# Optimization experiments

Hardware: AMD Instinct MI355X
Metric: run time of the kernel (lower is better)

Reference implementation:

```python
import jax, jax.numpy as jnp
import numpy as np

HIDDEN = 1024
FFN = 4096
NUM_EXPERTS = 8
TOP_K = 2
BATCH, SEQ = 2, 2048


def setup_inputs() -> dict:
    key = jax.random.key(0)
    ks = jax.random.split(key, 6)
    s_h = 1.0 / np.sqrt(HIDDEN)
    s_f = 1.0 / np.sqrt(FFN)
    return {
        "hidden_states": jax.random.normal(ks[0], (BATCH, SEQ, HIDDEN), jnp.float32),
        "gate_w": jax.random.uniform(ks[1], (HIDDEN, NUM_EXPERTS), jnp.float32, -s_h, s_h),
        "gate_b": jax.random.uniform(ks[2], (NUM_EXPERTS,), jnp.float32, -s_h, s_h),
        "w1": jax.random.uniform(ks[3], (NUM_EXPERTS, HIDDEN, FFN), jnp.float32, -s_h, s_h),
        "w3": jax.random.uniform(ks[4], (NUM_EXPERTS, HIDDEN, FFN), jnp.float32, -s_h, s_h),
        "w2": jax.random.uniform(ks[5], (NUM_EXPERTS, FFN, HIDDEN), jnp.float32, -s_f, s_f),
    }


def reference(hidden_states, gate_w, gate_b, w1, w3, w2):
    B, S, D = hidden_states.shape
    T = B * S
    x = hidden_states.reshape(T, D)

    # Router: softmax in fp32, top-2, renormalize (matches torch source)
    logits = x @ gate_w + gate_b                       # [T, E]
    probs = jax.nn.softmax(logits.astype(jnp.float32), axis=-1)
    top_w, top_idx = jax.lax.top_k(probs, TOP_K)       # [T, 2]
    top_w = top_w / jnp.sum(top_w, axis=-1, keepdims=True)

    # Dense combine weights [T, E]: zero for unselected experts.
    combine = jnp.zeros((T, NUM_EXPERTS), jnp.float32)
    combine = combine.at[jnp.arange(T)[:, None], top_idx].set(top_w)
    combine = combine.astype(x.dtype)

    # Grouped SwiGLU expert MLPs (vectorized over experts, zero-weight tokens
    # contribute nothing after combine).
    h = jax.nn.silu(jnp.einsum('td,edf->tef', x, w1)) * jnp.einsum('td,edf->tef', x, w3)
    out_e = jnp.einsum('tef,efd->ted', h, w2)          # [T, E, D]
    out = jnp.einsum('ted,te->td', out_e, combine)     # weighted combine
    return out.reshape(B, S, D)
```

## Files before the change

### kernel.cpp

```cpp
#include <hip/hip_runtime.h>


#define NTOK 4096
#define HID  1024
#define FFN  4096
#define NE   8
#define CAP  10240
#define MAXT 72
#define MAXT256 40
#define NKT5 16

typedef __bf16 bf16x8 __attribute__((ext_vector_type(8)));
typedef float  f32x4  __attribute__((ext_vector_type(4)));

typedef __attribute__((address_space(3))) unsigned int       lds_uint;
typedef const __attribute__((address_space(1))) unsigned int glob_uint;

__device__ __forceinline__ unsigned short f2bf(float f) {
  union { float f; unsigned u; } v; v.f = f;
  return (unsigned short)((v.u + 0x7FFFu + ((v.u >> 16) & 1u)) >> 16);
}

__device__ __forceinline__ void gload16(const void* g, void* l) {
  __builtin_amdgcn_global_load_lds((glob_uint*)g, (lds_uint*)l, 16, 0, 0);
}

__global__ void k0_zero_cvt(const float* __restrict__ x,
                            unsigned short* __restrict__ xbf,
                            float* __restrict__ out,
                            int* __restrict__ counts) {
  int i = blockIdx.x * 256 + threadIdx.x;
  const float4* x4 = (const float4*)x;
  float4 v = x4[i];
  uint2 p;
  p.x = (unsigned)f2bf(v.x) | ((unsigned)f2bf(v.y) << 16);
  p.y = (unsigned)f2bf(v.z) | ((unsigned)f2bf(v.w) << 16);
  ((uint2*)xbf)[i] = p;
  ((float4*)out)[i] = make_float4(0.f, 0.f, 0.f, 0.f);
  if (i < NE) counts[i] = 0;
}

__global__ __launch_bounds__(256) void k1_transpose(
    const float* __restrict__ s0, unsigned short* __restrict__ d0,
    const float* __restrict__ s1, unsigned short* __restrict__ d1,
    int Rfull, int Cfull, int rg0, int cg0, int RW, int CW) {
  __shared__ unsigned short tile[64 * 72];
  int z = blockIdx.z;
  const float* src = (z < 8 ? s0 : s1) + (size_t)(z & 7) * Rfull * Cfull;
  unsigned short* dst = (z < 8 ? d0 : d1) + (size_t)(z & 7) * RW * CW;
  int c0 = blockIdx.x * 64;
  int r0 = blockIdx.y * 64;
  int t = threadIdx.x;
  int q = t >> 4, p = t & 15;

  const float4* s4 = (const float4*)(src + (size_t)(rg0 + r0 + 4 * q) * Cfull
                                     + cg0 + c0) + p;
  unsigned short v[4][4];
#pragma unroll
  for (int u = 0; u < 4; u++) {
    float4 xv = s4[(size_t)u * (Cfull >> 2)];
    v[u][0] = f2bf(xv.x); v[u][1] = f2bf(xv.y);
    v[u][2] = f2bf(xv.z); v[u][3] = f2bf(xv.w);
  }
#pragma unroll
  for (int j = 0; j < 4; j++) {
    ushort4 w = make_ushort4(v[0][j], v[1][j], v[2][j], v[3][j]);
    *(ushort4*)&tile[(4 * p + j) * 72 + 4 * q] = w;
  }
  __syncthreads();
  int b = t & 7;
#pragma unroll
  for (int vi = 0; vi < 2; vi++) {
    int c = (t >> 3) + 32 * vi;
    uint4 w = *(const uint4*)&tile[c * 72 + 8 * b];
    *(uint4*)(dst + (size_t)(c0 + c) * RW + r0 + 8 * b) = w;
  }
}

__global__ void k2_router(const float* __restrict__ x,
                          const float* __restrict__ gw,
                          const float* __restrict__ gb,
                          int* __restrict__ topi, float* __restrict__ topw,
                          int* __restrict__ counts) {
  int wid = threadIdx.x >> 6, lane = threadIdx.x & 63;
  int t = blockIdx.x * 4 + wid;
  const float4* x4 = (const float4*)(x + (size_t)t * HID);
  const float4* g4 = (const float4*)gw;
  float acc[8];
#pragma unroll
  for (int e = 0; e < 8; e++) acc[e] = 0.f;
#pragma unroll
  for (int i = 0; i < 4; i++) {
    float4 xv = x4[i * 64 + lane];
    int dbase = (i * 64 + lane) * 4;
    float xs[4] = {xv.x, xv.y, xv.z, xv.w};
#pragma unroll
    for (int j = 0; j < 4; j++) {
      float4 ga  = g4[(dbase + j) * 2];
      float4 gbv = g4[(dbase + j) * 2 + 1];
      acc[0] += xs[j] * ga.x;  acc[1] += xs[j] * ga.y;
      acc[2] += xs[j] * ga.z;  acc[3] += xs[j] * ga.w;
      acc[4] += xs[j] * gbv.x; acc[5] += xs[j] * gbv.y;
      acc[6] += xs[j] * gbv.z; acc[7] += xs[j] * gbv.w;
    }
  }
#pragma unroll
  for (int e = 0; e < 8; e++)
#pragma unroll
    for (int m = 1; m < 64; m <<= 1) acc[e] += __shfl_xor(acc[e], m);
  if (lane == 0) {
    float lg[8];
#pragma unroll
    for (int e = 0; e < 8; e++) lg[e] = acc[e] + gb[e];
    int i0 = 0; float m0 = lg[0];
#pragma unroll
    for (int e = 1; e < 8; e++) if (lg[e] > m0) { m0 = lg[e]; i0 = e; }
    int i1 = -1; float m1 = -1e30f;
#pragma unroll
    for (int e = 0; e < 8; e++) if (e != i0 && lg[e] > m1) { m1 = lg[e]; i1 = e; }
    float w0 = 1.f / (1.f + __expf(m1 - m0));
    topi[2 * t] = i0; topi[2 * t + 1] = i1;
    topw[2 * t] = w0; topw[2 * t + 1] = 1.f - w0;
    atomicAdd(&counts[i0], 1);
    atomicAdd(&counts[i1], 1);
  }
}

__global__ void k3_scan(const int* __restrict__ counts, int* offs, int* fill,
                        int* t128_e, int* t128_row, int* t256_e, int* t256_row,
                        int* sorted_tok, float* sorted_w) {
  if (threadIdx.x == 0) {
    int off = 0, t1 = 0, t2 = 0;
    for (int e = 0; e < NE; e++) {
      offs[e] = off; fill[e] = 0;
      int nt1 = (counts[e] + 127) >> 7;
      for (int j = 0; j < nt1; j++) { t128_e[t1] = e; t128_row[t1] = off + j * 128; t1++; }
      int nt2 = (counts[e] + 255) >> 8;
      for (int j = 0; j < nt2; j++) { t256_e[t2] = e; t256_row[t2] = off + j * 256; t2++; }
      off += nt2 * 256;
    }
    for (; t1 < MAXT; t1++)    { t128_e[t1] = -1; t128_row[t1] = 0; }
    for (; t2 < MAXT256; t2++) { t256_e[t2] = -1; t256_row[t2] = 0; }
  }
  for (int i = threadIdx.x; i < CAP; i += 256) { sorted_tok[i] = 0; sorted_w[i] = 0.f; }
}

__global__ void k4_scatter(const int* __restrict__ topi, const float* __restrict__ topw,
                           const int* __restrict__ offs, int* __restrict__ fill,
                           int* __restrict__ sorted_tok, float* __restrict__ sorted_w) {
  int t = blockIdx.x * 256 + threadIdx.x;
#pragma unroll
  for (int k = 0; k < 2; k++) {
    int e = topi[2 * t + k];
    int p = atomicAdd(&fill[e], 1);
    int s = offs[e] + p;
    sorted_tok[s] = t;
    sorted_w[s]   = topw[2 * t + k];
  }
}


#define STG2(SMN, HOFF, S0, S1, KN)                        \
  do {                                                     \
    gload16((S0) + (KN), (SMN) + (HOFF) + sd);             \
    gload16((S1) + (KN), (SMN) + (HOFF) + 4096u + sd);     \
  } while (0)

template<int CFC>
__global__ __launch_bounds__(512, 2) void k5_gemm_h8(
    const unsigned short* __restrict__ xbf,
    const unsigned short* __restrict__ w1t,
    const unsigned short* __restrict__ w3t,
    unsigned short* __restrict__ h,
    const int* __restrict__ t256_e, const int* __restrict__ t256_row,
    const int* __restrict__ sorted_tok, int FCdyn) {
  const int FC = CFC ? CFC : FCdyn;
  extern __shared__ unsigned short sm[];

  int nb  = gridDim.x;
  int bid = blockIdx.x;
  int nid = (bid & 7) * (nb >> 3) + (bid >> 3);
  int tile = nid % MAXT256;
  int nblk = nid / MAXT256;

  int e = t256_e[tile];
  if (e < 0) return;
  int row0 = t256_row[tile];
  int n0 = nblk * 128;
  int tid = threadIdx.x;

  int sr = tid >> 3;
  int cs = ((tid & 7) ^ (sr & 7)) * 8;
  const unsigned short* pA0 = xbf + (size_t)sorted_tok[row0 +       sr] * HID + cs;
  const unsigned short* pA1 = xbf + (size_t)sorted_tok[row0 +  64 + sr] * HID + cs;
  const unsigned short* pA2 = xbf + (size_t)sorted_tok[row0 + 128 + sr] * HID + cs;
  const unsigned short* pA3 = xbf + (size_t)sorted_tok[row0 + 192 + sr] * HID + cs;
  size_t rb0 = ((size_t)e * FC + n0 + sr) * HID + cs;
  size_t rb1 = rb0 + (size_t)64 * HID;
  const unsigned short* pB10 = w1t + rb0;
  const unsigned short* pB11 = w1t + rb1;
  const unsigned short* pB30 = w3t + rb0;
  const unsigned short* pB31 = w3t + rb1;
  unsigned sd = (unsigned)tid * 8u;

  int wid = tid >> 6, lane = tid & 63, lm = lane & 15, q = lane >> 4;
  int wr = wid >> 1, wc = wid & 1;
  unsigned aOff  = (unsigned)(wr * 64 + lm) * 64u;
  unsigned b1Off = 16384u + (unsigned)(wc * 64 + lm) * 64u;
  unsigned b3Off = 24576u + (unsigned)(wc * 64 + lm) * 64u;
  unsigned px0 = (unsigned)((q ^ (lm & 7)) * 8);
  unsigned px1 = (unsigned)(((4 + q) ^ (lm & 7)) * 8);

  f32x4 acc1[4][4] = {};
  f32x4 acc3[4][4] = {};
  bf16x8 af[4][2], bfr[2][2];

  {
    unsigned short* smn = sm;
    STG2(smn, 0u,     pA0,  pA1,  0);
    STG2(smn, 8192u,  pA2,  pA3,  0);
    STG2(smn, 16384u, pB10, pB11, 0);
    STG2(smn, 24576u, pB30, pB31, 0);
  }
  asm volatile("s_waitcnt vmcnt(2)" ::: "memory");
  __builtin_amdgcn_s_barrier();
  __builtin_amdgcn_sched_barrier(0);

#pragma unroll 1
  for (int kt = 0; kt < NKT5; kt++) {
    const unsigned short* smc = sm + ((kt & 1) ? 32768u : 0u);
    unsigned short*       smn = sm + ((kt & 1) ? 0u : 32768u);
    int kn = ((kt + 1) & (NKT5 - 1)) * 64;

#pragma unroll
    for (int ti = 0; ti < 4; ti++) {
      af[ti][0] = *(const bf16x8*)(smc + aOff + ti * 1024u + px0);
      af[ti][1] = *(const bf16x8*)(smc + aOff + ti * 1024u + px1);
    }
#pragma unroll
    for (int j = 0; j < 2; j++) {
      bfr[j][0] = *(const bf16x8*)(smc + b1Off + j * 1024u + px0);
      bfr[j][1] = *(const bf16x8*)(smc + b1Off + j * 1024u + px1);
    }
    STG2(smn, 0u, pA0, pA1, kn);
    __builtin_amdgcn_s_barrier();
    __builtin_amdgcn_sched_barrier(0);
    __builtin_amdgcn_s_setprio(1);
#pragma unroll
    for (int ti = 0; ti < 4; ti++)
#pragma unroll
      for (int j = 0; j < 2; j++) {
        acc1[ti][j] = __builtin_amdgcn_mfma_f32_16x16x32_bf16(af[ti][0], bfr[j][0], acc1[ti][j], 0, 0, 0);
        acc1[ti][j] = __builtin_amdgcn_mfma_f32_16x16x32_bf16(af[ti][1], bfr[j][1], acc1[ti][j], 0, 0, 0);
      }
    __builtin_amdgcn_s_setprio(0);

#pragma unroll
    for (int j = 0; j < 2; j++) {
      bfr[j][0] = *(const bf16x8*)(smc + b1Off + 2048u + j * 1024u + px0);
      bfr[j][1] = *(const bf16x8*)(smc + b1Off + 2048u + j * 1024u + px1);
    }
    STG2(smn, 8192u, pA2, pA3, kn);
    asm volatile("s_waitcnt vmcnt(4)" ::: "memory");
    __builtin_amdgcn_s_barrier();
    __builtin_amdgcn_sched_barrier(0);
    __builtin_amdgcn_s_setprio(1);
#pragma unroll
    for (int ti = 0; ti < 4; ti++)
#pragma unroll
      for (int j = 0; j < 2; j++) {
        acc1[ti][2 + j] = __builtin_amdgcn_mfma_f32_16x16x32_bf16(af[ti][0], bfr[j][0], acc1[ti][2 + j], 0, 0, 0);
        acc1[ti][2 + j] = __builtin_amdgcn_mfma_f32_16x16x32_bf16(af[ti][1], bfr[j][1], acc1[ti][2 + j], 0, 0, 0);
      }
    __builtin_amdgcn_s_setprio(0);

#pragma unroll
    for (int j = 0; j < 2; j++) {
      bfr[j][0] = *(const bf16x8*)(smc + b3Off + j * 1024u + px0);
      bfr[j][1] = *(const bf16x8*)(smc + b3Off + j * 1024u + px1);
    }
    STG2(smn, 16384u, pB10, pB11, kn);
    __builtin_amdgcn_s_barrier();
    __builtin_amdgcn_sched_barrier(0);
    __builtin_amdgcn_s_setprio(1);
#pragma unroll
    for (int ti = 0; ti < 4; ti++)
#pragma unroll
      for (int j = 0; j < 2; j++) {
        acc3[ti][j] = __builtin_amdgcn_mfma_f32_16x16x32_bf16(af[ti][0], bfr[j][0], acc3[ti][j], 0, 0, 0);
        acc3[ti][j] = __builtin_amdgcn_mfma_f32_16x16x32_bf16(af[ti][1], bfr[j][1], acc3[ti][j], 0, 0, 0);
      }
    __builtin_amdgcn_s_setprio(0);

#pragma unroll
    for (int j = 0; j < 2; j++) {
      bfr[j][0] = *(const bf16x8*)(smc + b3Off + 2048u + j * 1024u + px0);
      bfr[j][1] = *(const bf16x8*)(smc + b3Off + 2048u + j * 1024u + px1);
    }
    STG2(smn, 24576u, pB30, pB31, kn);
    asm volatile("s_waitcnt vmcnt(2)" ::: "memory");
    __builtin_amdgcn_s_barrier();
    __builtin_amdgcn_sched_barrier(0);
    __builtin_amdgcn_s_setprio(1);
#pragma unroll
    for (int ti = 0; ti < 4; ti++)
#pragma unroll
      for (int j = 0; j < 2; j++) {
        acc3[ti][2 + j] = __builtin_amdgcn_mfma_f32_16x16x32_bf16(af[ti][0], bfr[j][0], acc3[ti][2 + j], 0, 0, 0);
        acc3[ti][2 + j] = __builtin_amdgcn_mfma_f32_16x16x32_bf16(af[ti][1], bfr[j][1], acc3[ti][2 + j], 0, 0, 0);
      }
    __builtin_amdgcn_s_setprio(0);
  }
  asm volatile("s_waitcnt vmcnt(0)" ::: "memory");

#pragma unroll
  for (int ti = 0; ti < 4; ti++)
#pragma unroll
    for (int tj = 0; tj < 4; tj++)
#pragma unroll
      for (int r = 0; r < 4; r++) {
        float v1 = acc1[ti][tj][r];
        float v3 = acc3[ti][tj][r];
        float hv = (v1 / (1.f + __expf(-v1))) * v3;
        int grow = row0 + wr * 64 + ti * 16 + q * 4 + r;
        int gcol = n0 + wc * 64 + tj * 16 + lm;
        h[(size_t)grow * FC + gcol] = f2bf(hv);
      }
}

template<int CFC>
__global__ __launch_bounds__(256) void k6_gemm_out(
    const unsigned short* __restrict__ h,
    const unsigned short* __restrict__ w2t,
    float* __restrict__ out,
    const int* __restrict__ tile_e, const int* __restrict__ tile_row,
    const int* __restrict__ sorted_tok, const float* __restrict__ sorted_w,
    int FCdyn) {
  const int FC = CFC ? CFC : FCdyn;
  __shared__ unsigned short lsA[128 * 32];
  __shared__ unsigned short lsB[128 * 32];
  __shared__ int   toks[128];
  __shared__ float wts[128];

  int nbk  = (int)(gridDim.x * gridDim.y);
  int bidl = (int)(blockIdx.x + gridDim.x * blockIdx.y);
  int nidk = (bidl & 7) * (nbk >> 3) + (bidl >> 3);
  int tile = nidk % (int)gridDim.x;
  int yb   = nidk / (int)gridDim.x;

  int e = tile_e[tile];
  if (e < 0) return;
  int row0 = tile_row[tile];
  int n0 = yb * 128;
  int tid = threadIdx.x;

  if (tid < 128) { toks[tid] = sorted_tok[row0 + tid]; wts[tid] = sorted_w[row0 + tid]; }

  int kc = tid & 3, lr = tid >> 2;
  int g = (kc ^ ((lr >> 1) & 3)) * 8;
  const unsigned short* ga0 = h + (size_t)(row0 + lr) * FC + g;
  const unsigned short* ga1 = h + (size_t)(row0 + lr + 64) * FC + g;
  const unsigned short* gb0 = w2t + ((size_t)e * HID + n0 + lr) * FC + g;
  const unsigned short* gb1 = w2t + ((size_t)e * HID + n0 + lr + 64) * FC + g;
  unsigned short* la0 = lsA + tid * 8;
  unsigned short* la1 = lsA + (256 + tid) * 8;
  unsigned short* lb0 = lsB + tid * 8;
  unsigned short* lb1 = lsB + (256 + tid) * 8;

  int wid = tid >> 6, lane = tid & 63, lm = lane & 15, q = lane >> 4;
  int wr = wid >> 1, wc = wid & 1;
  int qs = (q ^ ((lm >> 1) & 3)) * 8;
  const unsigned short* As = lsA + (wr * 64 + lm) * 32 + qs;
  const unsigned short* Bs = lsB + (wc * 64 + lm) * 32 + qs;

  f32x4 acc[4][4] = {};

#pragma unroll 1
  for (int ks = 0; ks < FC / 32; ks++) {
    __syncthreads();
    int k0 = ks * 32;
    gload16(ga0 + k0, la0);
    gload16(ga1 + k0, la1);
    gload16(gb0 + k0, lb0);
    gload16(gb1 + k0, lb1);
    __syncthreads();
    bf16x8 a[4], b[4];
#pragma unroll
    for (int ti = 0; ti < 4; ti++) a[ti] = *(const bf16x8*)(As + ti * 512);
#pragma unroll
    for (int tj = 0; tj < 4; tj++) b[tj] = *(const bf16x8*)(Bs + tj * 512);
#pragma unroll
    for (int ti = 0; ti < 4; ti++)
#pragma unroll
      for (int tj = 0; tj < 4; tj++)
        acc[ti][tj] = __builtin_amdgcn_mfma_f32_16x16x32_bf16(a[ti], b[tj], acc[ti][tj], 0, 0, 0);
  }

#pragma unroll
  for (int ti = 0; ti < 4; ti++)
#pragma unroll
    for (int r = 0; r < 4; r++) {
      int lrow = wr * 64 + ti * 16 + q * 4 + r;
      float wt = wts[lrow];
      if (wt != 0.f) {
        int trow = toks[lrow];
#pragma unroll
        for (int tj = 0; tj < 4; tj++) {
          int gcol = n0 + wc * 64 + tj * 16 + lm;
          atomicAdd(&out[(size_t)trow * HID + gcol], acc[ti][tj][r] * wt);
        }
      }
    }
}

extern "C" void kernel_launch(void* const* d_in, const int* in_sizes, int n_in,
                              void* d_out, int out_size, void* d_ws, size_t ws_size,
                              hipStream_t stream) {
  const float* x  = (const float*)d_in[0];
  const float* gw = (const float*)d_in[1];
  const float* gb = (const float*)d_in[2];
  const float* w1 = (const float*)d_in[3];
  const float* w3 = (const float*)d_in[4];
  const float* w2 = (const float*)d_in[5];
  float* out = (float*)d_out;

  char* ws = (char*)d_ws;
  int*   counts     = (int*)(ws + 0);
  int*   fill       = (int*)(ws + 32);
  int*   offs       = (int*)(ws + 64);
  int*   t128_e     = (int*)(ws + 96);
  int*   t128_row   = (int*)(ws + 416);
  int*   t256_e     = (int*)(ws + 736);
  int*   t256_row   = (int*)(ws + 896);
  int*   topi       = (int*)(ws + 2048);
  float* topw       = (float*)(ws + 34816);
  int*   sorted_tok = (int*)(ws + 67584);
  float* sorted_w   = (float*)(ws + 108544);
  unsigned short* xbf = (unsigned short*)(ws + 149504);
  const size_t base = 8538112ull;

  int FC = FFN;
  while (FC > 128) {
    size_t W  = (size_t)NE * FC * HID * 2;
    size_t Hb = (size_t)CAP * FC * 2;
    if (base + 3 * W + Hb <= ws_size) break;
    FC >>= 1;
  }
  size_t W = (size_t)NE * FC * HID * 2;
  unsigned short* w1t  = (unsigned short*)(ws + base);
  unsigned short* w3t  = (unsigned short*)(ws + base + W);
  unsigned short* w2t  = (unsigned short*)(ws + base + 2 * W);
  unsigned short* hbuf = (unsigned short*)(ws + base + 3 * W);
  int nc = FFN / FC;

  static bool attr_set = false;
  if (!attr_set) {
    hipFuncSetAttribute((const void*)k5_gemm_h8<4096>, hipFuncAttributeMaxDynamicSharedMemorySize, 131072);
    hipFuncSetAttribute((const void*)k5_gemm_h8<2048>, hipFuncAttributeMaxDynamicSharedMemorySize, 131072);
    hipFuncSetAttribute((const void*)k5_gemm_h8<1024>, hipFuncAttributeMaxDynamicSharedMemorySize, 131072);
    hipFuncSetAttribute((const void*)k5_gemm_h8<0>,    hipFuncAttributeMaxDynamicSharedMemorySize, 131072);
    attr_set = true;
  }

  k0_zero_cvt<<<4096, 256, 0, stream>>>(x, xbf, out, counts);
  k2_router<<<1024, 256, 0, stream>>>(x, gw, gb, topi, topw, counts);
  k3_scan<<<1, 256, 0, stream>>>(counts, offs, fill, t128_e, t128_row,
                                 t256_e, t256_row, sorted_tok, sorted_w);
  k4_scatter<<<16, 256, 0, stream>>>(topi, topw, offs, fill, sorted_tok, sorted_w);

  for (int c = 0; c < nc; c++) {
    int c0 = c * FC;
    k1_transpose<<<dim3(FC / 64, HID / 64, 16), 256, 0, stream>>>(
        w1, w1t, w3, w3t, HID, FFN, 0, c0, HID, FC);
    k1_transpose<<<dim3(HID / 64, FC / 64, 8), 256, 0, stream>>>(
        w2, w2t, nullptr, nullptr, FFN, HID, c0, 0, FC, HID);
    dim3 g5(MAXT256 * (FC / 128));
    if (FC == 4096) {
      k5_gemm_h8<4096><<<g5, 512, 131072, stream>>>(
          xbf, w1t, w3t, hbuf, t256_e, t256_row, sorted_tok, FC);
      k6_gemm_out<4096><<<dim3(MAXT, HID / 128), 256, 0, stream>>>(
          hbuf, w2t, out, t128_e, t128_row, sorted_tok, sorted_w, FC);
    } else if (FC == 2048) {
      k5_gemm_h8<2048><<<g5, 512, 131072, stream>>>(
          xbf, w1t, w3t, hbuf, t256_e, t256_row, sorted_tok, FC);
      k6_gemm_out<2048><<<dim3(MAXT, HID / 128), 256, 0, stream>>>(
          hbuf, w2t, out, t128_e, t128_row, sorted_tok, sorted_w, FC);
    } else if (FC == 1024) {
      k5_gemm_h8<1024><<<g5, 512, 131072, stream>>>(
          xbf, w1t, w3t, hbuf, t256_e, t256_row, sorted_tok, FC);
      k6_gemm_out<1024><<<dim3(MAXT, HID / 128), 256, 0, stream>>>(
          hbuf, w2t, out, t128_e, t128_row, sorted_tok, sorted_w, FC);
    } else {
      k5_gemm_h8<0><<<g5, 512, 131072, stream>>>(
          xbf, w1t, w3t, hbuf, t256_e, t256_row, sorted_tok, FC);
      k6_gemm_out<0><<<dim3(MAXT, HID / 128), 256, 0, stream>>>(
          hbuf, w2t, out, t128_e, t128_row, sorted_tok, sorted_w, FC);
    }
  }
}
```

Measured before the change: 871.1 us.

## Rewrite down-projection GEMM as 256x256 double-buffered 8-wave pipelined kernel

Replaces the 128x128 single-buffered down-projection kernel with a 512-thread kernel that computes a 256-row by 256-column output tile. It reuses the k5 style: double-buffered LDS in 64-wide K steps, staged global-to-LDS loads interleaved with MFMA phases, and setprio around the MFMA blocks. Each wave owns two 128-column halves through two accumulator sets. The aim is more data reuse per loaded byte and overlap of memory loads with MFMA work, at the cost of higher register and LDS use (128KB dynamic) and coarser tiles. Routing tables with 256-row tiles can waste more work on padded rows.

```diff
diff --git a/kernel.cpp b/kernel.cpp
--- a/kernel.cpp
+++ b/kernel.cpp
@@ -329,72 +329,155 @@
 }
 
 template<int CFC>
-__global__ __launch_bounds__(256) void k6_gemm_out(
+__global__ __launch_bounds__(512, 2) void k6_gemm_o8(
     const unsigned short* __restrict__ h,
     const unsigned short* __restrict__ w2t,
     float* __restrict__ out,
-    const int* __restrict__ tile_e, const int* __restrict__ tile_row,
+    const int* __restrict__ t256_e, const int* __restrict__ t256_row,
     const int* __restrict__ sorted_tok, const float* __restrict__ sorted_w,
     int FCdyn) {
   const int FC = CFC ? CFC : FCdyn;
-  __shared__ unsigned short lsA[128 * 32];
-  __shared__ unsigned short lsB[128 * 32];
-  __shared__ int   toks[128];
-  __shared__ float wts[128];
-
-  int nbk  = (int)(gridDim.x * gridDim.y);
-  int bidl = (int)(blockIdx.x + gridDim.x * blockIdx.y);
-  int nidk = (bidl & 7) * (nbk >> 3) + (bidl >> 3);
-  int tile = nidk % (int)gridDim.x;
-  int yb   = nidk / (int)gridDim.x;
-
-  int e = tile_e[tile];
+  const int NKT = FC / 64;
+  extern __shared__ unsigned short sm[];
+  __shared__ int   toks[256];
+  __shared__ float wts[256];
+
+  int nb  = gridDim.x;
+  int bid = blockIdx.x;
+  int nid = (bid & 7) * (nb >> 3) + (bid >> 3);
+  int tile = nid % MAXT256;
+  int nblk = nid / MAXT256;
+
+  int e = t256_e[tile];
   if (e < 0) return;
-  int row0 = tile_row[tile];
-  int n0 = yb * 128;
+  int row0 = t256_row[tile];
+  int n0 = nblk * 256;
   int tid = threadIdx.x;
 
-  if (tid < 128) { toks[tid] = sorted_tok[row0 + tid]; wts[tid] = sorted_w[row0 + tid]; }
-
-  int kc = tid & 3, lr = tid >> 2;
-  int g = (kc ^ ((lr >> 1) & 3)) * 8;
-  const unsigned short* ga0 = h + (size_t)(row0 + lr) * FC + g;
-  const unsigned short* ga1 = h + (size_t)(row0 + lr + 64) * FC + g;
-  const unsigned short* gb0 = w2t + ((size_t)e * HID + n0 + lr) * FC + g;
-  const unsigned short* gb1 = w2t + ((size_t)e * HID + n0 + lr + 64) * FC + g;
-  unsigned short* la0 = lsA + tid * 8;
-  unsigned short* la1 = lsA + (256 + tid) * 8;
-  unsigned short* lb0 = lsB + tid * 8;
-  unsigned short* lb1 = lsB + (256 + tid) * 8;
+  if (tid < 256) { toks[tid] = sorted_tok[row0 + tid]; wts[tid] = sorted_w[row0 + tid]; }
+
+  int sr = tid >> 3;
+  int cs = ((tid & 7) ^ (sr & 7)) * 8;
+  const unsigned short* pA0 = h + (size_t)(row0 +       sr) * FC + cs;
+  const unsigned short* pA1 = h + (size_t)(row0 +  64 + sr) * FC + cs;
+  const unsigned short* pA2 = h + (size_t)(row0 + 128 + sr) * FC + cs;
+  const unsigned short* pA3 = h + (size_t)(row0 + 192 + sr) * FC + cs;
+  size_t rb = ((size_t)e * HID + n0 + sr) * FC + cs;
+  const unsigned short* pB10 = w2t + rb;
+  const unsigned short* pB11 = w2t + rb + (size_t)64  * FC;
+  const unsigned short* pB30 = w2t + rb + (size_t)128 * FC;
+  const unsigned short* pB31 = w2t + rb + (size_t)192 * FC;
+  unsigned sd = (unsigned)tid * 8u;
 
   int wid = tid >> 6, lane = tid & 63, lm = lane & 15, q = lane >> 4;
   int wr = wid >> 1, wc = wid & 1;
-  int qs = (q ^ ((lm >> 1) & 3)) * 8;
-  const unsigned short* As = lsA + (wr * 64 + lm) * 32 + qs;
-  const unsigned short* Bs = lsB + (wc * 64 + lm) * 32 + qs;
-
-  f32x4 acc[4][4] = {};
+  unsigned aOff  = (unsigned)(wr * 64 + lm) * 64u;
+  unsigned b1Off = 16384u + (unsigned)(wc * 64 + lm) * 64u;
+  unsigned b3Off = 24576u + (unsigned)(wc * 64 + lm) * 64u;
+  unsigned px0 = (unsigned)((q ^ (lm & 7)) * 8);
+  unsigned px1 = (unsigned)(((4 + q) ^ (lm & 7)) * 8);
+
+  f32x4 acc1[4][4] = {};
+  f32x4 acc3[4][4] = {};
+  bf16x8 af[4][2], bfr[2][2];
+
+  {
+    unsigned short* smn = sm;
+    STG2(smn, 0u,     pA0,  pA1,  0);
+    STG2(smn, 8192u,  pA2,  pA3,  0);
+    STG2(smn, 16384u, pB10, pB11, 0);
+    STG2(smn, 24576u, pB30, pB31, 0);
+  }
+  asm volatile("s_waitcnt vmcnt(2)" ::: "memory");
+  __builtin_amdgcn_s_barrier();
+  __builtin_amdgcn_sched_barrier(0);
 
 #pragma unroll 1
-  for (int ks = 0; ks < FC / 32; ks++) {
-    __syncthreads();
-    int k0 = ks * 32;
-    gload16(ga0 + k0, la0);
-    gload16(ga1 + k0, la1);
-    gload16(gb0 + k0, lb0);
-    gload16(gb1 + k0, lb1);
-    __syncthreads();
-    bf16x8 a[4], b[4];
-#pragma unroll
-    for (int ti = 0; ti < 4; ti++) a[ti] = *(const bf16x8*)(As + ti * 512);
-#pragma unroll
-    for (int tj = 0; tj < 4; tj++) b[tj] = *(const bf16x8*)(Bs + tj * 512);
-#pragma unroll
-    for (int ti = 0; ti < 4; ti++)
-#pragma unroll
-      for (int tj = 0; tj < 4; tj++)
-        acc[ti][tj] = __builtin_amdgcn_mfma_f32_16x16x32_bf16(a[ti], b[tj], acc[ti][tj], 0, 0, 0);
-  }
+  for (int kt = 0; kt < NKT; kt++) {
+    const unsigned short* smc = sm + ((kt & 1) ? 32768u : 0u);
+    unsigned short*       smn = sm + ((kt & 1) ? 0u : 32768u);
+    int kn = (kt + 1 == NKT ? 0 : kt + 1) * 64;
+
+#pragma unroll
+    for (int ti = 0; ti < 4; ti++) {
+      af[ti][0] = *(const bf16x8*)(smc + aOff + ti * 1024u + px0);
+      af[ti][1] = *(const bf16x8*)(smc + aOff + ti * 1024u + px1);
+    }
+#pragma unroll
+    for (int j = 0; j < 2; j++) {
+      bfr[j][0] = *(const bf16x8*)(smc + b1Off + j * 1024u + px0);
+      bfr[j][1] = *(const bf16x8*)(smc + b1Off + j * 1024u + px1);
+    }
+    STG2(smn, 0u, pA0, pA1, kn);
+    __builtin_amdgcn_s_barrier();
+    __builtin_amdgcn_sched_barrier(0);
+    __builtin_amdgcn_s_setprio(1);
+#pragma unroll
+    for (int ti = 0; ti < 4; ti++)
+#pragma unroll
+      for (int j = 0; j < 2; j++) {
+        acc1[ti][j] = __builtin_amdgcn_mfma_f32_16x16x32_bf16(af[ti][0], bfr[j][0], acc1[ti][j], 0, 0, 0);
+        acc1[ti][j] = __builtin_amdgcn_mfma_f32_16x16x32_bf16(af[ti][1], bfr[j][1], acc1[ti][j], 0, 0, 0);
+      }
+    __builtin_amdgcn_s_setprio(0);
+
+#pragma unroll
+    for (int j = 0; j < 2; j++) {
+      bfr[j][0] = *(const bf16x8*)(smc + b1Off + 2048u + j * 1024u + px0);
+      bfr[j][1] = *(const bf16x8*)(smc + b1Off + 2048u + j * 1024u + px1);
+    }
+    STG2(smn, 8192u, pA2, pA3, kn);
+    asm volatile("s_waitcnt vmcnt(4)" ::: "memory");
+    __builtin_amdgcn_s_barrier();
+    __builtin_amdgcn_sched_barrier(0);
+    __builtin_amdgcn_s_setprio(1);
+#pragma unroll
+    for (int ti = 0; ti < 4; ti++)
+#pragma unroll
+      for (int j = 0; j < 2; j++) {
+        acc1[ti][2 + j] = __builtin_amdgcn_mfma_f32_16x16x32_bf16(af[ti][0], bfr[j][0], acc1[ti][2 + j], 0, 0, 0);
+        acc1[ti][2 + j] = __builtin_amdgcn_mfma_f32_16x16x32_bf16(af[ti][1], bfr[j][1], acc1[ti][2 + j], 0, 0, 0);
+      }
+    __builtin_amdgcn_s_setprio(0);
+
+#pragma unroll
+    for (int j = 0; j < 2; j++) {
+      bfr[j][0] = *(const bf16x8*)(smc + b3Off + j * 1024u + px0);
+      bfr[j][1] = *(const bf16x8*)(smc + b3Off + j * 1024u + px1);
+    }
+    STG2(smn, 16384u, pB10, pB11, kn);
+    __builtin_amdgcn_s_barrier();
+    __builtin_amdgcn_sched_barrier(0);
+    __builtin_amdgcn_s_setprio(1);
+#pragma unroll
+    for (int ti = 0; ti < 4; ti++)
+#pragma unroll
+      for (int j = 0; j < 2; j++) {
+        acc3[ti][j] = __builtin_amdgcn_mfma_f32_16x16x32_bf16(af[ti][0], bfr[j][0], acc3[ti][j], 0, 0, 0);
+        acc3[ti][j] = __builtin_amdgcn_mfma_f32_16x16x32_bf16(af[ti][1], bfr[j][1], acc3[ti][j], 0, 0, 0);
+      }
+    __builtin_amdgcn_s_setprio(0);
+
+#pragma unroll
+    for (int j = 0; j < 2; j++) {
+      bfr[j][0] = *(const bf16x8*)(smc + b3Off + 2048u + j * 1024u + px0);
+      bfr[j][1] = *(const bf16x8*)(smc + b3Off + 2048u + j * 1024u + px1);
+    }
+    STG2(smn, 24576u, pB30, pB31, kn);
+    asm volatile("s_waitcnt vmcnt(2)" ::: "memory");
+    __builtin_amdgcn_s_barrier();
+    __builtin_amdgcn_sched_barrier(0);
+    __builtin_amdgcn_s_setprio(1);
+#pragma unroll
+    for (int ti = 0; ti < 4; ti++)
+#pragma unroll
+      for (int j = 0; j < 2; j++) {
+        acc3[ti][2 + j] = __builtin_amdgcn_mfma_f32_16x16x32_bf16(af[ti][0], bfr[j][0], acc3[ti][2 + j], 0, 0, 0);
+        acc3[ti][2 + j] = __builtin_amdgcn_mfma_f32_16x16x32_bf16(af[ti][1], bfr[j][1], acc3[ti][2 + j], 0, 0, 0);
+      }
+    __builtin_amdgcn_s_setprio(0);
+  }
+  asm volatile("s_waitcnt vmcnt(0)" ::: "memory");
 
 #pragma unroll
   for (int ti = 0; ti < 4; ti++)
@@ -407,7 +490,8 @@
 #pragma unroll
         for (int tj = 0; tj < 4; tj++) {
           int gcol = n0 + wc * 64 + tj * 16 + lm;
-          atomicAdd(&out[(size_t)trow * HID + gcol], acc[ti][tj][r] * wt);
+          atomicAdd(&out[(size_t)trow * HID + gcol],       acc1[ti][tj][r] * wt);
+          atomicAdd(&out[(size_t)trow * HID + gcol + 128], acc3[ti][tj][r] * wt);
         }
       }
     }
@@ -459,6 +543,10 @@
     hipFuncSetAttribute((const void*)k5_gemm_h8<2048>, hipFuncAttributeMaxDynamicSharedMemorySize, 131072);
     hipFuncSetAttribute((const void*)k5_gemm_h8<1024>, hipFuncAttributeMaxDynamicSharedMemorySize, 131072);
     hipFuncSetAttribute((const void*)k5_gemm_h8<0>,    hipFuncAttributeMaxDynamicSharedMemorySize, 131072);
+    hipFuncSetAttribute((const void*)k6_gemm_o8<4096>, hipFuncAttributeMaxDynamicSharedMemorySize, 131072);
+    hipFuncSetAttribute((const void*)k6_gemm_o8<2048>, hipFuncAttributeMaxDynamicSharedMemorySize, 131072);
+    hipFuncSetAttribute((const void*)k6_gemm_o8<1024>, hipFuncAttributeMaxDynamicSharedMemorySize, 131072);
+    hipFuncSetAttribute((const void*)k6_gemm_o8<0>,    hipFuncAttributeMaxDynamicSharedMemorySize, 131072);
     attr_set = true;
   }
 
@@ -475,26 +563,27 @@
     k1_transpose<<<dim3(HID / 64, FC / 64, 8), 256, 0, stream>>>(
         w2, w2t, nullptr, nullptr, FFN, HID, c0, 0, FC, HID);
     dim3 g5(MAXT256 * (FC / 128));
+    dim3 g6(MAXT256 * (HID / 256));
     if (FC == 4096) {
       k5_gemm_h8<4096><<<g5, 512, 131072, stream>>>(
           xbf, w1t, w3t, hbuf, t256_e, t256_row, sorted_tok, FC);
-      k6_gemm_out<4096><<<dim3(MAXT, HID / 128), 256, 0, stream>>>(
-          hbuf, w2t, out, t128_e, t128_row, sorted_tok, sorted_w, FC);
+      k6_gemm_o8<4096><<<g6, 512, 131072, stream>>>(
+          hbuf, w2t, out, t256_e, t256_row, sorted_tok, sorted_w, FC);
     } else if (FC == 2048) {
       k5_gemm_h8<2048><<<g5, 512, 131072, stream>>>(
           xbf, w1t, w3t, hbuf, t256_e, t256_row, sorted_tok, FC);
-      k6_gemm_out<2048><<<dim3(MAXT, HID / 128), 256, 0, stream>>>(
-          hbuf, w2t, out, t128_e, t128_row, sorted_tok, sorted_w, FC);
+      k6_gemm_o8<2048><<<g6, 512, 131072, stream>>>(
+          hbuf, w2t, out, t256_e, t256_row, sorted_tok, sorted_w, FC);
     } else if (FC == 1024) {
       k5_gemm_h8<1024><<<g5, 512, 131072, stream>>>(
           xbf, w1t, w3t, hbuf, t256_e, t256_row, sorted_tok, FC);
-      k6_gemm_out<1024><<<dim3(MAXT, HID / 128), 256, 0, stream>>>(
-          hbuf, w2t, out, t128_e, t128_row, sorted_tok, sorted_w, FC);
+      k6_gemm_o8<1024><<<g6, 512, 131072, stream>>>(
+          hbuf, w2t, out, t256_e, t256_row, sorted_tok, sorted_w, FC);
     } else {
       k5_gemm_h8<0><<<g5, 512, 131072, stream>>>(
           xbf, w1t, w3t, hbuf, t256_e, t256_row, sorted_tok, FC);
-      k6_gemm_out<0><<<dim3(MAXT, HID / 128), 256, 0, stream>>>(
-          hbuf, w2t, out, t128_e, t128_row, sorted_tok, sorted_w, FC);
-    }
-  }
-}
+      k6_gemm_o8<0><<<g6, 512, 131072, stream>>>(
+          hbuf, w2t, out, t256_e, t256_row, sorted_tok, sorted_w, FC);
+    }
+  }
+}
```

New measurement: 838.4 us. 3.8% less time.
